# Kernel optimization log

Measured on AMD Instinct MI355X. Metric: run time of the kernel, lower is better.

## Reference

```python
import jax, jax.numpy as jnp
import numpy as np

B = 4000        # graphs
N = 64          # atoms (nodes) per graph; also conv1 in_channels (Linear(num_atoms, 64))
C = 64          # hidden / out channels (hard-coded 64 in ChargeModel)
E_PER = 512     # edges per graph (avg degree 8)
NT = B * N      # total nodes


def setup_inputs() -> dict:
    key = jax.random.key(0)
    ks = jax.random.split(key, 10)
    x = jax.random.normal(ks[0], (NT, N), dtype=jnp.float32)
    # block-local random edges: each graph's edges stay inside its node block
    off = (jnp.arange(B, dtype=jnp.int32) * N)[:, None]
    src = (jax.random.randint(ks[1], (B, E_PER), 0, N, dtype=jnp.int32) + off).reshape(-1)
    dst = (jax.random.randint(ks[2], (B, E_PER), 0, N, dtype=jnp.int32) + off).reshape(-1)
    edge_index = jnp.stack([src, dst], axis=0)  # [2, B*E_PER]
    s = 1.0 / jnp.sqrt(jnp.float32(C))  # keep activations O(1) across 3 layers
    W1 = jax.random.normal(ks[3], (N, C), dtype=jnp.float32) * s
    W2 = jax.random.normal(ks[4], (C, C), dtype=jnp.float32) * s
    W3 = jax.random.normal(ks[5], (C, C), dtype=jnp.float32) * s
    b1 = jax.random.normal(ks[6], (C,), dtype=jnp.float32) * 0.1
    b2 = jax.random.normal(ks[7], (C,), dtype=jnp.float32) * 0.1
    b3 = jax.random.normal(ks[8], (C,), dtype=jnp.float32) * 0.1
    return {"x": x, "edge_index": edge_index, "W1": W1, "b1": b1,
            "W2": W2, "b2": b2, "W3": W3, "b3": b3}


def reference(x, edge_index, W1, b1, W2, b2, W3, b3):
    nt = x.shape[0]
    src, dst = edge_index[0], edge_index[1]
    loops = jnp.arange(nt, dtype=src.dtype)
    row = jnp.concatenate([src, loops])  # self-loops appended (add_self_loops)
    col = jnp.concatenate([dst, loops])
    # degree of target nodes (col), shared across the three layers
    deg = jax.ops.segment_sum(jnp.ones(row.shape[0], dtype=x.dtype), col, num_segments=nt)
    dinv = jnp.where(deg > 0, jax.lax.rsqrt(jnp.maximum(deg, 1e-12)), 0.0)
    norm = dinv[row] * dinv[col]  # [E']

    def gcn(h, W, b):
        h = h @ W                                   # linear (no bias in lin)
        msg = norm[:, None] * h[row]                # message: norm * x_j
        out = jax.ops.segment_sum(msg, col, num_segments=nt)  # aggr='add'
        return out + b

    h = gcn(x, W1, b1)
    h = gcn(h, W2, b2)
    h = gcn(h, W3, b3)
    # per-graph readout: mean over nodes and channels -> one scalar per graph
    y = h.reshape(B, N, C).mean(axis=(1, 2))
    return y
```

## Files before the change

kernel.cpp:

```cpp
#include <hip/hip_runtime.h>

#define NG      4000
#define EPG     512
#define CSTRIDE 36

__device__ inline float dot4(const float4 a, const float4 b) {
    return a.x * b.x + a.y * b.y + a.z * b.z + a.w * b.w;
}

__global__ __launch_bounds__(256) void prep_vec(
    const float* __restrict__ W1, const float* __restrict__ b1,
    const float* __restrict__ W2, const float* __restrict__ b2,
    const float* __restrict__ W3, const float* __restrict__ b3,
    float* __restrict__ out)
{
    __shared__ float w3[64], q2[64];
    const int t  = threadIdx.x;
    const int rg = t >> 4;
    const int l16 = t & 15;

    const float4* W1_4 = (const float4*)W1;
    const float4* W2_4 = (const float4*)W2;
    const float4* W3_4 = (const float4*)W3;
    float4 a3[4], a2[4], a1[4];
    #pragma unroll
    for (int j = 0; j < 4; ++j) a3[j] = W3_4[t + 256 * j];
    #pragma unroll
    for (int j = 0; j < 4; ++j) a2[j] = W2_4[t + 256 * j];
    #pragma unroll
    for (int j = 0; j < 4; ++j) a1[j] = W1_4[t + 256 * j];
    float bb1 = 0.f, bb2 = 0.f, bb3 = 0.f;
    if (t < 64) { bb1 = b1[t]; bb2 = b2[t]; bb3 = b3[t]; }

    #pragma unroll
    for (int j = 0; j < 4; ++j) {
        float s = a3[j].x + a3[j].y + a3[j].z + a3[j].w;
        s += __shfl_down(s, 8, 16);
        s += __shfl_down(s, 4, 16);
        s += __shfl_down(s, 2, 16);
        s += __shfl_down(s, 1, 16);
        if (l16 == 0) w3[16 * j + rg] = s;
    }
    __syncthreads();

    {
        const float4 wc = ((const float4*)w3)[l16];
        #pragma unroll
        for (int j = 0; j < 4; ++j) {
            float s = dot4(a2[j], wc);
            s += __shfl_down(s, 8, 16);
            s += __shfl_down(s, 4, 16);
            s += __shfl_down(s, 2, 16);
            s += __shfl_down(s, 1, 16);
            if (l16 == 0) q2[16 * j + rg] = s;
        }
    }
    __syncthreads();

    {
        const float4 qc = ((const float4*)q2)[l16];
        #pragma unroll
        for (int j = 0; j < 4; ++j) {
            float s = dot4(a1[j], qc);
            s += __shfl_down(s, 8, 16);
            s += __shfl_down(s, 4, 16);
            s += __shfl_down(s, 2, 16);
            s += __shfl_down(s, 1, 16);
            if (l16 == 0) out[16 * j + rg] = s;
        }
    }

    if (t < 64) {
        float t1 = bb1 * q2[t];
        float t2 = bb2 * w3[t];
        float t3 = bb3;
        #pragma unroll
        for (int off = 32; off > 0; off >>= 1) {
            t1 += __shfl_down(t1, off, 64);
            t2 += __shfl_down(t2, off, 64);
            t3 += __shfl_down(t3, off, 64);
        }
        if (t == 0) { out[64] = t1; out[65] = t2; out[66] = 64.f * t3; }
    }
}

__global__ __launch_bounds__(256, 8) void gcn3_collapse3(
    const float* __restrict__ x, const int* __restrict__ ei,
    const float* __restrict__ pv, float* __restrict__ y, int etot)
{
    __shared__ int   Cnt[64 * CSTRIDE];
    __shared__ int   deg4[4][64];
    __shared__ float dinv[64], zdA[64], zdB[64], u1[64], u2[64], u3[64], xp[64];

    const int g = blockIdx.x, t = threadIdx.x;
    const int w = t >> 6;
    const int base = g * 64;
    const int row = t >> 2, q4 = t & 3;

    const float4* xg = (const float4*)(x + (size_t)g * 4096 + row * 64 + q4 * 16);
    const float4 xr0 = xg[0], xr1 = xg[1], xr2 = xg[2], xr3 = xg[3];

    const int2 sv = *(const int2*)(ei + (size_t)g * EPG + 2 * t);
    const int2 dv = *(const int2*)(ei + (size_t)etot + (size_t)g * EPG + 2 * t);

    const float4* pp = (const float4*)(pv + q4 * 16);
    const float4 p0 = pp[0], p1 = pp[1], p2 = pp[2], p3 = pp[3];

    {
        const int4 z = {0, 0, 0, 0};
        int4* c4 = (int4*)Cnt;
        #pragma unroll 1
        for (int i = t; i < (64 * CSTRIDE) / 4; i += 256) c4[i] = z;
        ((int*)deg4)[t] = 0;
    }
    __syncthreads();

    {
        const int sa = sv.x - base, da = dv.x - base;
        const int sb = sv.y - base, db = dv.y - base;
        atomicAdd(&deg4[w][da], 1);
        atomicAdd(&deg4[w][db], 1);
        atomicAdd(&Cnt[sa * CSTRIDE + (da >> 1)], 1 << ((da & 1) * 16));
        atomicAdd(&Cnt[sb * CSTRIDE + (db >> 1)], 1 << ((db & 1) * 16));
    }

    {
        float part = dot4(xr0, p0) + dot4(xr1, p1) + dot4(xr2, p2) + dot4(xr3, p3);
        part += __shfl_down(part, 2, 4);
        part += __shfl_down(part, 1, 4);
        if (q4 == 0) xp[row] = part;
    }
    __syncthreads();

    if (t < 64) {
        const int ds = deg4[0][t] + deg4[1][t] + deg4[2][t] + deg4[3][t];
        const float di = rsqrtf((float)(ds + 1));
        dinv[t] = di;
        zdA[t] = di;
    }
    __syncthreads();

    auto upass = [&](const float* zin, float* zout, const float* uprev, float* u) {
        const int4* rp = (const int4*)(Cnt + row * CSTRIDE + q4 * 8);
        const int4 c0 = rp[0], c1 = rp[1];
        const float4* zp = (const float4*)(zin + q4 * 16);
        const float4 z0 = zp[0], z1 = zp[1], z2 = zp[2], z3 = zp[3];
        float acc = 0.f;
        acc += (float)((unsigned)c0.x & 0xffffu) * z0.x + (float)((unsigned)c0.x >> 16) * z0.y;
        acc += (float)((unsigned)c0.y & 0xffffu) * z0.z + (float)((unsigned)c0.y >> 16) * z0.w;
        acc += (float)((unsigned)c0.z & 0xffffu) * z1.x + (float)((unsigned)c0.z >> 16) * z1.y;
        acc += (float)((unsigned)c0.w & 0xffffu) * z1.z + (float)((unsigned)c0.w >> 16) * z1.w;
        acc += (float)((unsigned)c1.x & 0xffffu) * z2.x + (float)((unsigned)c1.x >> 16) * z2.y;
        acc += (float)((unsigned)c1.y & 0xffffu) * z2.z + (float)((unsigned)c1.y >> 16) * z2.w;
        acc += (float)((unsigned)c1.z & 0xffffu) * z3.x + (float)((unsigned)c1.z >> 16) * z3.y;
        acc += (float)((unsigned)c1.w & 0xffffu) * z3.z + (float)((unsigned)c1.w >> 16) * z3.w;
        acc += __shfl_down(acc, 2, 4);
        acc += __shfl_down(acc, 1, 4);
        if (q4 == 0) {
            const float di = dinv[row];
            const float zp_ = uprev ? uprev[row] : 1.0f;
            const float uv = di * acc + di * di * zp_;
            u[row] = uv;
            if (zout) zout[row] = di * uv;
        }
        __syncthreads();
    };

    upass(zdA, zdB, nullptr, u1);
    upass(zdB, zdA, u1,      u2);
    upass(zdA, nullptr, u2,  u3);

    if (t < 64) {
        float r  = u3[t] * xp[t];
        float a1 = u1[t];
        float a2 = u2[t];
        #pragma unroll
        for (int off = 32; off > 0; off >>= 1) {
            r  += __shfl_down(r,  off, 64);
            a1 += __shfl_down(a1, off, 64);
            a2 += __shfl_down(a2, off, 64);
        }
        if (t == 0) {
            const float beta1 = pv[64], beta2 = pv[65], beta3 = pv[66];
            y[g] = (r + a2 * beta1 + a1 * beta2 + beta3) * (1.0f / 4096.0f);
        }
    }
}

extern "C" void kernel_launch(void* const* d_in, const int* in_sizes, int n_in,
                              void* d_out, int out_size, void* d_ws, size_t ws_size,
                              hipStream_t stream) {
    const float* x  = (const float*)d_in[0];
    const int*   ei = (const int*)  d_in[1];
    const float* W1 = (const float*)d_in[2];
    const float* b1 = (const float*)d_in[3];
    const float* W2 = (const float*)d_in[4];
    const float* b2 = (const float*)d_in[5];
    const float* W3 = (const float*)d_in[6];
    const float* b3 = (const float*)d_in[7];
    float* y = (float*)d_out;
    const int etot = in_sizes[1] / 2;

    float* pv = (float*)d_ws;
    hipLaunchKernelGGL(prep_vec, dim3(1), dim3(256), 0, stream,
                       W1, b1, W2, b2, W3, b3, pv);
    hipLaunchKernelGGL(gcn3_collapse3, dim3(NG), dim3(256), 0, stream,
                       x, ei, pv, y, etot);
}
```

Measured before the change: 23.52 us.

## Fuse weight-collapse prep into main kernel and interleave with graph passes

```diff
diff --git a/kernel.cpp b/kernel.cpp
--- a/kernel.cpp
+++ b/kernel.cpp
@@ -8,94 +8,24 @@
     return a.x * b.x + a.y * b.y + a.z * b.z + a.w * b.w;
 }
 
-__global__ __launch_bounds__(256) void prep_vec(
+__global__ __launch_bounds__(256, 6) void gcn3_one(
+    const float* __restrict__ x, const int* __restrict__ ei,
     const float* __restrict__ W1, const float* __restrict__ b1,
     const float* __restrict__ W2, const float* __restrict__ b2,
     const float* __restrict__ W3, const float* __restrict__ b3,
-    float* __restrict__ out)
-{
-    __shared__ float w3[64], q2[64];
-    const int t  = threadIdx.x;
-    const int rg = t >> 4;
-    const int l16 = t & 15;
-
-    const float4* W1_4 = (const float4*)W1;
-    const float4* W2_4 = (const float4*)W2;
-    const float4* W3_4 = (const float4*)W3;
-    float4 a3[4], a2[4], a1[4];
-    #pragma unroll
-    for (int j = 0; j < 4; ++j) a3[j] = W3_4[t + 256 * j];
-    #pragma unroll
-    for (int j = 0; j < 4; ++j) a2[j] = W2_4[t + 256 * j];
-    #pragma unroll
-    for (int j = 0; j < 4; ++j) a1[j] = W1_4[t + 256 * j];
-    float bb1 = 0.f, bb2 = 0.f, bb3 = 0.f;
-    if (t < 64) { bb1 = b1[t]; bb2 = b2[t]; bb3 = b3[t]; }
-
-    #pragma unroll
-    for (int j = 0; j < 4; ++j) {
-        float s = a3[j].x + a3[j].y + a3[j].z + a3[j].w;
-        s += __shfl_down(s, 8, 16);
-        s += __shfl_down(s, 4, 16);
-        s += __shfl_down(s, 2, 16);
-        s += __shfl_down(s, 1, 16);
-        if (l16 == 0) w3[16 * j + rg] = s;
-    }
-    __syncthreads();
-
-    {
-        const float4 wc = ((const float4*)w3)[l16];
-        #pragma unroll
-        for (int j = 0; j < 4; ++j) {
-            float s = dot4(a2[j], wc);
-            s += __shfl_down(s, 8, 16);
-            s += __shfl_down(s, 4, 16);
-            s += __shfl_down(s, 2, 16);
-            s += __shfl_down(s, 1, 16);
-            if (l16 == 0) q2[16 * j + rg] = s;
-        }
-    }
-    __syncthreads();
-
-    {
-        const float4 qc = ((const float4*)q2)[l16];
-        #pragma unroll
-        for (int j = 0; j < 4; ++j) {
-            float s = dot4(a1[j], qc);
-            s += __shfl_down(s, 8, 16);
-            s += __shfl_down(s, 4, 16);
-            s += __shfl_down(s, 2, 16);
-            s += __shfl_down(s, 1, 16);
-            if (l16 == 0) out[16 * j + rg] = s;
-        }
-    }
-
-    if (t < 64) {
-        float t1 = bb1 * q2[t];
-        float t2 = bb2 * w3[t];
-        float t3 = bb3;
-        #pragma unroll
-        for (int off = 32; off > 0; off >>= 1) {
-            t1 += __shfl_down(t1, off, 64);
-            t2 += __shfl_down(t2, off, 64);
-            t3 += __shfl_down(t3, off, 64);
-        }
-        if (t == 0) { out[64] = t1; out[65] = t2; out[66] = 64.f * t3; }
-    }
-}
-
-__global__ __launch_bounds__(256, 8) void gcn3_collapse3(
-    const float* __restrict__ x, const int* __restrict__ ei,
-    const float* __restrict__ pv, float* __restrict__ y, int etot)
+    float* __restrict__ y, int etot)
 {
     __shared__ int   Cnt[64 * CSTRIDE];
     __shared__ int   deg4[4][64];
-    __shared__ float dinv[64], zdA[64], zdB[64], u1[64], u2[64], u3[64], xp[64];
+    __shared__ float w3S[64], q2S[64], pS[64];
+    __shared__ float dinvS[64], zdA[64], zdB[64];
+    __shared__ float u1S[64], u2S[64], u3S[64], xpS[64];
+    __shared__ float betaS[3];
 
-    const int g = blockIdx.x, t = threadIdx.x;
-    const int w = t >> 6;
+    const int g = blockIdx.x, t = threadIdx.x, w = t >> 6;
     const int base = g * 64;
-    const int row = t >> 2, q4 = t & 3;
+    const int row = t >> 2,  q4  = t & 3;
+    const int rg  = t >> 4,  l16 = t & 15;
 
     const float4* xg = (const float4*)(x + (size_t)g * 4096 + row * 64 + q4 * 16);
     const float4 xr0 = xg[0], xr1 = xg[1], xr2 = xg[2], xr3 = xg[3];
@@ -103,14 +33,20 @@
     const int2 sv = *(const int2*)(ei + (size_t)g * EPG + 2 * t);
     const int2 dv = *(const int2*)(ei + (size_t)etot + (size_t)g * EPG + 2 * t);
 
-    const float4* pp = (const float4*)(pv + q4 * 16);
-    const float4 p0 = pp[0], p1 = pp[1], p2 = pp[2], p3 = pp[3];
+    const float4* W3_4 = (const float4*)W3;
+    const float4* W2_4 = (const float4*)W2;
+    const float4* W1_4 = (const float4*)W1;
+    float4 aW[4];
+    #pragma unroll
+    for (int j = 0; j < 4; ++j) aW[j] = W3_4[t + 256 * j];
+    float bb1 = 0.f, bb2 = 0.f, bb3 = 0.f;
+    if (t < 64) { bb1 = b1[t]; bb2 = b2[t]; bb3 = b3[t]; }
 
     {
         const int4 z = {0, 0, 0, 0};
         int4* c4 = (int4*)Cnt;
-        #pragma unroll 1
-        for (int i = t; i < (64 * CSTRIDE) / 4; i += 256) c4[i] = z;
+        c4[t] = z; c4[t + 256] = z;
+        if (t < 64) c4[t + 512] = z;
         ((int*)deg4)[t] = 0;
     }
     __syncthreads();
@@ -123,21 +59,39 @@
         atomicAdd(&Cnt[sa * CSTRIDE + (da >> 1)], 1 << ((da & 1) * 16));
         atomicAdd(&Cnt[sb * CSTRIDE + (db >> 1)], 1 << ((db & 1) * 16));
     }
-
-    {
-        float part = dot4(xr0, p0) + dot4(xr1, p1) + dot4(xr2, p2) + dot4(xr3, p3);
-        part += __shfl_down(part, 2, 4);
-        part += __shfl_down(part, 1, 4);
-        if (q4 == 0) xp[row] = part;
+    #pragma unroll
+    for (int j = 0; j < 4; ++j) {
+        float s = aW[j].x + aW[j].y + aW[j].z + aW[j].w;
+        s += __shfl_down(s, 8, 16);
+        s += __shfl_down(s, 4, 16);
+        s += __shfl_down(s, 2, 16);
+        s += __shfl_down(s, 1, 16);
+        if (l16 == 0) w3S[16 * j + rg] = s;
     }
+    #pragma unroll
+    for (int j = 0; j < 4; ++j) aW[j] = W2_4[t + 256 * j];
     __syncthreads();
 
     if (t < 64) {
         const int ds = deg4[0][t] + deg4[1][t] + deg4[2][t] + deg4[3][t];
         const float di = rsqrtf((float)(ds + 1));
-        dinv[t] = di;
+        dinvS[t] = di;
         zdA[t] = di;
     }
+    {
+        const float4 wc = ((const float4*)w3S)[l16];
+        #pragma unroll
+        for (int j = 0; j < 4; ++j) {
+            float s = dot4(aW[j], wc);
+            s += __shfl_down(s, 8, 16);
+            s += __shfl_down(s, 4, 16);
+            s += __shfl_down(s, 2, 16);
+            s += __shfl_down(s, 1, 16);
+            if (l16 == 0) q2S[16 * j + rg] = s;
+        }
+    }
+    #pragma unroll
+    for (int j = 0; j < 4; ++j) aW[j] = W1_4[t + 256 * j];
     __syncthreads();
 
     auto upass = [&](const float* zin, float* zout, const float* uprev, float* u) {
@@ -157,23 +111,59 @@
         acc += __shfl_down(acc, 2, 4);
         acc += __shfl_down(acc, 1, 4);
         if (q4 == 0) {
-            const float di = dinv[row];
+            const float di = dinvS[row];
             const float zp_ = uprev ? uprev[row] : 1.0f;
             const float uv = di * acc + di * di * zp_;
             u[row] = uv;
             if (zout) zout[row] = di * uv;
         }
-        __syncthreads();
     };
 
-    upass(zdA, zdB, nullptr, u1);
-    upass(zdB, zdA, u1,      u2);
-    upass(zdA, nullptr, u2,  u3);
+    upass(zdA, zdB, nullptr, u1S);
+    {
+        const float4 qc = ((const float4*)q2S)[l16];
+        #pragma unroll
+        for (int j = 0; j < 4; ++j) {
+            float s = dot4(aW[j], qc);
+            s += __shfl_down(s, 8, 16);
+            s += __shfl_down(s, 4, 16);
+            s += __shfl_down(s, 2, 16);
+            s += __shfl_down(s, 1, 16);
+            if (l16 == 0) pS[16 * j + rg] = s;
+        }
+    }
+    if (t < 64) {
+        float t1 = bb1 * q2S[t];
+        float t2 = bb2 * w3S[t];
+        float t3 = bb3;
+        #pragma unroll
+        for (int off = 32; off > 0; off >>= 1) {
+            t1 += __shfl_down(t1, off, 64);
+            t2 += __shfl_down(t2, off, 64);
+            t3 += __shfl_down(t3, off, 64);
+        }
+        if (t == 0) { betaS[0] = t1; betaS[1] = t2; betaS[2] = 64.f * t3; }
+    }
+    __syncthreads();
+
+    upass(zdB, zdA, u1S, u2S);
+    {
+        const float4* pp4 = (const float4*)(pS + q4 * 16);
+        float part = dot4(xr0, pp4[0]) + dot4(xr1, pp4[1])
+                   + dot4(xr2, pp4[2]) + dot4(xr3, pp4[3]);
+        part += __shfl_down(part, 2, 4);
+        part += __shfl_down(part, 1, 4);
+        if (q4 == 0) xpS[row] = part;
+    }
+    __syncthreads();
+
+    upass(zdA, nullptr, u2S, u3S);
+    __syncthreads();
 
     if (t < 64) {
-        float r  = u3[t] * xp[t];
-        float a1 = u1[t];
-        float a2 = u2[t];
+        float r  = u3S[t] * xpS[t];
+        float a1 = u1S[t];
+        float a2 = u2S[t];
         #pragma unroll
         for (int off = 32; off > 0; off >>= 1) {
             r  += __shfl_down(r,  off, 64);
@@ -181,8 +171,7 @@
             a2 += __shfl_down(a2, off, 64);
         }
         if (t == 0) {
-            const float beta1 = pv[64], beta2 = pv[65], beta3 = pv[66];
-            y[g] = (r + a2 * beta1 + a1 * beta2 + beta3) * (1.0f / 4096.0f);
+            y[g] = (r + a2 * betaS[0] + a1 * betaS[1] + betaS[2]) * (1.0f / 4096.0f);
         }
     }
 }
@@ -201,9 +190,6 @@
     float* y = (float*)d_out;
     const int etot = in_sizes[1] / 2;
 
-    float* pv = (float*)d_ws;
-    hipLaunchKernelGGL(prep_vec, dim3(1), dim3(256), 0, stream,
-                       W1, b1, W2, b2, W3, b3, pv);
-    hipLaunchKernelGGL(gcn3_collapse3, dim3(NG), dim3(256), 0, stream,
-                       x, ei, pv, y, etot);
+    hipLaunchKernelGGL(gcn3_one, dim3(NG), dim3(256), 0, stream,
+                       x, ei, W1, b1, W2, b2, W3, b3, y, etot);
 }
```

Measured after the change: 29.09 us. 1.24x slower.
